# Kernel optimization log

Measured on AMD Instinct MI355X. Metric: run time of the kernel, lower is better.

## Reference

```python
import jax, jax.numpy as jnp
import numpy as np

B, L, D, H = 4, 2048, 2048, 16
HD = D // H
ROPE_BASE = 10000.0


def _rope_cos_sin(seq_len, dim):
    # torchtune-style: theta_i = base^{-2i/dim}, angles[t, i] = t * theta_i
    inv_freq = 1.0 / (ROPE_BASE ** (jnp.arange(0, dim, 2, dtype=jnp.float32) / dim))  # [dim/2]
    angles = jnp.arange(seq_len, dtype=jnp.float32)[:, None] * inv_freq[None, :]  # [L, dim/2]
    return jnp.cos(angles), jnp.sin(angles)


def _apply_rope(x, cos, sin):
    # x: [B, L, H, hd]; rotate interleaved pairs (x0, x1)
    x1 = x[..., 0::2]  # [B, L, H, hd/2]
    x2 = x[..., 1::2]
    c = cos[None, :, None, :]
    s = sin[None, :, None, :]
    o1 = x1 * c - x2 * s
    o2 = x2 * c + x1 * s
    return jnp.stack([o1, o2], axis=-1).reshape(x.shape)


def setup_inputs() -> dict:
    key = jax.random.key(0)
    k1, k2, k3 = jax.random.split(key, 3)
    x = jax.random.normal(k1, (B, L, D), dtype=jnp.float32)
    w_qkv = jax.random.normal(k2, (3 * D, D), dtype=jnp.float32) * (D ** -0.5)
    w_o = jax.random.normal(k3, (D, D), dtype=jnp.float32) * (D ** -0.5)
    return {"x": x, "w_qkv": w_qkv, "w_o": w_o}


def reference(x, w_qkv, w_o):
    qkv = jnp.einsum("bld,ed->ble", x, w_qkv)  # [B, L, 3D]
    q, k, v = jnp.split(qkv, 3, axis=-1)
    q = q.reshape(B, L, H, HD)
    k = k.reshape(B, L, H, HD)
    v = v.reshape(B, L, H, HD)
    cos, sin = _rope_cos_sin(L, HD)
    q = _apply_rope(q, cos, sin)
    k = _apply_rope(k, cos, sin)
    # [B, H, L, hd]
    q = q.transpose(0, 2, 1, 3)
    k = k.transpose(0, 2, 1, 3)
    v = v.transpose(0, 2, 1, 3)
    scores = jnp.einsum("bhqd,bhkd->bhqk", q, k) * (HD ** -0.5)
    causal = jnp.tril(jnp.ones((L, L), dtype=bool))
    scores = jnp.where(causal[None, None], scores, jnp.finfo(scores.dtype).min)
    attn = jax.nn.softmax(scores, axis=-1)
    y = jnp.einsum("bhqk,bhkd->bhqd", attn, v)
    y = y.transpose(0, 2, 1, 3).reshape(B, L, D)
    return jnp.einsum("bld,ed->ble", y, w_o)
```

## Files before the change

### kernel.cpp

```cpp
#include <hip/hip_runtime.h>

#define L_SEQ 2048
#define DMODEL 2048
#define NHEAD 16
#define HDIM 128
#define BATCH 4

typedef _Float16 f16x8 __attribute__((ext_vector_type(8)));
typedef _Float16 f16x4 __attribute__((ext_vector_type(4)));
typedef float f32x4 __attribute__((ext_vector_type(4)));

__device__ __forceinline__ void gload16(const void* g, void* l) {
  __builtin_amdgcn_global_load_lds((const __attribute__((address_space(1))) void*)g,
                                   (__attribute__((address_space(3))) void*)l, 16, 0, 0);
}

__global__ __launch_bounds__(256) void cvt_blocked(const float* __restrict__ in,
                                                   _Float16* __restrict__ out, int K) {
  const int kt = blockIdx.x, mb = blockIdx.y, KT = K >> 6;
  const int t = threadIdx.x, row = t >> 1, half = t & 1;
  const float* src = in + (size_t)(mb * 128 + row) * K + kt * 64 + half * 32;
  _Float16* tile = out + ((size_t)mb * KT + kt) * 8192;
  for (int j = 0; j < 4; ++j) {
    float4 a = *(const float4*)(src + j * 8);
    float4 b = *(const float4*)(src + j * 8 + 4);
    f16x8 o;
    o[0] = (_Float16)a.x; o[1] = (_Float16)a.y; o[2] = (_Float16)a.z; o[3] = (_Float16)a.w;
    o[4] = (_Float16)b.x; o[5] = (_Float16)b.y; o[6] = (_Float16)b.z; o[7] = (_Float16)b.w;
    int kb = half * 4 + j;
    *(f16x8*)(tile + (size_t)(kb * 128 + row) * 8) = o;
  }
}

template <typename OUT>
__global__ __launch_bounds__(256, 4) void gemm_bt(const _Float16* __restrict__ A,
                                                  const _Float16* __restrict__ Bt,
                                                  OUT* __restrict__ C,
                                                  int M, int N, int K) {
  __shared__ _Float16 As[2][128 * 64];
  __shared__ _Float16 Bs[2][128 * 64];
  const int KT = K >> 6;
  const int tid = threadIdx.x;
  const int wave = tid >> 6, lane = tid & 63, quad = lane >> 4, l15 = lane & 15;
  const int xcd = blockIdx.x & 7;
  const int lm = blockIdx.x >> 3;
  const int tm = xcd * 8 + (lm & 7);
  const int tn = lm >> 3;
  if (tm * 128 >= M || tn * 128 >= N) return;
  const int wm = (wave >> 1) * 64, wn = (wave & 1) * 64;
  const int id = wave * 4;
  const _Float16* tA0 = A + (size_t)tm * KT * 8192;
  const _Float16* tB0 = Bt + (size_t)tn * KT * 8192;

  auto stage = [&](int kt, int buf) {
    const _Float16* tA = tA0 + (size_t)kt * 8192;
    const _Float16* tB = tB0 + (size_t)kt * 8192;
    for (int j = 0; j < 4; ++j) {
      gload16(tA + (size_t)(id + j) * 512 + lane * 8, (char*)As[buf] + (id + j) * 1024);
      gload16(tB + (size_t)(id + j) * 512 + lane * 8, (char*)Bs[buf] + (id + j) * 1024);
    }
  };

  f32x4 acc[4][4] = {};
  stage(0, 0);
  int cur = 0;
  for (int kt = 0; kt < KT; ++kt) {
    const bool more = (kt + 1) < KT;
    if (more) {
      stage(kt + 1, cur ^ 1);
      asm volatile("s_waitcnt vmcnt(8)" ::: "memory");
    } else {
      asm volatile("s_waitcnt vmcnt(0)" ::: "memory");
    }
    __builtin_amdgcn_sched_barrier(0);
    __builtin_amdgcn_s_barrier();
    const f16x8* A8 = (const f16x8*)As[cur];
    const f16x8* B8 = (const f16x8*)Bs[cur];
    __builtin_amdgcn_s_setprio(1);
    for (int kk = 0; kk < 2; ++kk) {
      int kb = kk * 4 + quad;
      f16x8 af[4], bf[4];
      for (int mi = 0; mi < 4; ++mi) af[mi] = A8[kb * 128 + wm + mi * 16 + l15];
      for (int ni = 0; ni < 4; ++ni) bf[ni] = B8[kb * 128 + wn + ni * 16 + l15];
      for (int mi = 0; mi < 4; ++mi)
        for (int ni = 0; ni < 4; ++ni)
          acc[mi][ni] = __builtin_amdgcn_mfma_f32_16x16x32_f16(af[mi], bf[ni], acc[mi][ni], 0, 0, 0);
    }
    __builtin_amdgcn_s_setprio(0);
    asm volatile("s_waitcnt lgkmcnt(0)" ::: "memory");
    __builtin_amdgcn_sched_barrier(0);
    __builtin_amdgcn_s_barrier();
    cur ^= 1;
  }
  for (int mi = 0; mi < 4; ++mi)
    for (int ni = 0; ni < 4; ++ni) {
      int r = tm * 128 + wm + mi * 16 + quad * 4;
      int c = tn * 128 + wn + ni * 16 + l15;
      for (int reg = 0; reg < 4; ++reg)
        C[(size_t)(r + reg) * N + c] = (OUT)acc[mi][ni][reg];
    }
}

__global__ void rope_scatter(const _Float16* __restrict__ qkv,
                             _Float16* __restrict__ qt,
                             _Float16* __restrict__ kt) {
  int row = blockIdx.x;
  int pe = blockIdx.y * 256 + threadIdx.x;
  int e = pe * 2;
  float x1 = (float)qkv[(size_t)row * 6144 + e];
  float x2 = (float)qkv[(size_t)row * 6144 + e + 1];
  int which = e >> 11;
  int h = (e >> 7) & 15;
  int hd = e & 127;
  int b = row >> 11, l = row & 2047;
  int bh = b * 16 + h;
  int i = hd >> 1;
  float ang = (float)l * __expf((float)i * -0.14391156831212787f);
  float s, c;
  __sincosf(ang, &s, &c);
  float o1 = x1 * c - x2 * s;
  float o2 = x2 * c + x1 * s;
  _Float16* dst = (which == 0) ? qt : kt;
  size_t base = ((size_t)bh * 2048 + l) * 128 + hd;
  dst[base] = (_Float16)o1;
  dst[base + 1] = (_Float16)o2;
}

__global__ __launch_bounds__(256) void v_transpose(const _Float16* __restrict__ qkv,
                                                   _Float16* __restrict__ vt) {
  __shared__ _Float16 Ls[64 * 72];
  const int tid = threadIdx.x;
  const int l0 = blockIdx.x * 64;
  const int hd0 = blockIdx.y * 64;
  const int bh = blockIdx.z;
  const int b = bh >> 4, h = bh & 15;
  const size_t colbase = 4096 + h * 128 + hd0;
  for (int i = 0; i < 2; ++i) {
    int chunk = tid + i * 256;
    int r = chunk >> 3, c = chunk & 7;
    f16x8 v = *(const f16x8*)(qkv + (size_t)(b * 2048 + l0 + r) * 6144 + colbase + c * 8);
    *(f16x8*)(Ls + r * 72 + c * 8) = v;
  }
  __syncthreads();
  for (int i = 0; i < 2; ++i) {
    int chunk = tid + i * 256;
    int hr = chunk >> 3, c = chunk & 7;
    f16x8 o;
    for (int j = 0; j < 8; ++j) o[j] = Ls[(c * 8 + j) * 72 + hr];
    *(f16x8*)(vt + ((size_t)bh * 128 + hd0 + hr) * 2048 + l0 + c * 8) = o;
  }
}

__global__ __launch_bounds__(512, 4) void attn_fwd(const _Float16* __restrict__ qt,
                                                   const _Float16* __restrict__ kt,
                                                   const _Float16* __restrict__ vt,
                                                   _Float16* __restrict__ y) {
  __shared__ _Float16 Kl[64 * 128];
  __shared__ _Float16 Vl[64 * 128];
  __shared__ _Float16 Pl[8 * 16 * 64];
  const int a = blockIdx.y >> 2, bq = blockIdx.y & 3;
  const int qb = (a == 0) ? 15 - bq : (a == 1) ? 8 + bq : (a == 2) ? 4 + bq : 3 - bq;
  const int q0 = qb * 128;
  const int bh = blockIdx.x;
  const int tid = threadIdx.x;
  const int wave = tid >> 6, lane = tid & 63, quad = lane >> 4, l15 = lane & 15;
  const _Float16* Q = qt + (size_t)bh * L_SEQ * HDIM;
  const _Float16* Kg = kt + (size_t)bh * L_SEQ * HDIM;
  const _Float16* Vg = vt + (size_t)bh * HDIM * L_SEQ;

  const float scale = 0.08838834764831845f;
  f16x8 qf[4];
  {
    int qrow = q0 + wave * 16 + l15;
    const _Float16 hs = (_Float16)scale;
    for (int kk = 0; kk < 4; ++kk) {
      qf[kk] = *(const f16x8*)(Q + (size_t)qrow * 128 + kk * 32 + quad * 8);
      for (int j = 0; j < 8; ++j) qf[kk][j] *= hs;
    }
  }
  f32x4 o[8] = {};
  float mi[4] = {-1e30f, -1e30f, -1e30f, -1e30f};
  float li[4] = {0.f, 0.f, 0.f, 0.f};
  const int ntile = 2 * qb + 2;

  auto stageK = [&](int kv0) {
    for (int j = 0; j < 2; ++j) {
      int id = wave * 2 + j;
      gload16(Kg + (size_t)(kv0 + lane) * 128 + id * 8, (char*)Kl + id * 1024);
    }
  };
  auto stageV = [&](int kv0) {
    for (int j = 0; j < 2; ++j) {
      int id = wave * 2 + j;
      int kvb = id >> 1, h0 = (id & 1) * 64;
      gload16(Vg + (size_t)(h0 + lane) * L_SEQ + (kv0 + kvb * 8), (char*)Vl + (kvb * 128 + h0) * 16);
    }
  };

  stageK(0);
  stageV(0);

  for (int t = 0; t < ntile; ++t) {
    const int kv0 = t * 64;
    const bool more = (t + 1) < ntile;

    asm volatile("s_waitcnt vmcnt(2)" ::: "memory");
    __builtin_amdgcn_sched_barrier(0);
    __builtin_amdgcn_s_barrier();

    f32x4 s[4] = {};
    {
      const f16x8* K8 = (const f16x8*)Kl;
      __builtin_amdgcn_s_setprio(1);
      for (int kk = 0; kk < 4; ++kk) {
        int hb = kk * 4 + quad;
        for (int ni = 0; ni < 4; ++ni) {
          f16x8 bfr = K8[hb * 64 + ni * 16 + l15];
          s[ni] = __builtin_amdgcn_mfma_f32_16x16x32_f16(qf[kk], bfr, s[ni], 0, 0, 0);
        }
      }
      __builtin_amdgcn_s_setprio(0);
    }
    __builtin_amdgcn_sched_barrier(0);
    __builtin_amdgcn_s_barrier();
    __builtin_amdgcn_sched_barrier(0);
    if (more) stageK(kv0 + 64);

    float mx[4];
    if (t >= ntile - 2) {
      for (int reg = 0; reg < 4; ++reg) {
        int rowg = q0 + wave * 16 + quad * 4 + reg;
        float m = -1e30f;
        for (int ni = 0; ni < 4; ++ni) {
          float v = s[ni][reg];
          if ((kv0 + ni * 16 + l15) > rowg) v = -1e30f;
          s[ni][reg] = v;
          m = fmaxf(m, v);
        }
        mx[reg] = m;
      }
    } else {
      for (int reg = 0; reg < 4; ++reg)
        mx[reg] = fmaxf(fmaxf(s[0][reg], s[1][reg]), fmaxf(s[2][reg], s[3][reg]));
    }
    for (int off = 1; off < 16; off <<= 1)
      for (int reg = 0; reg < 4; ++reg)
        mx[reg] = fmaxf(mx[reg], __shfl_xor(mx[reg], off));
    float dm = fmaxf(fmaxf(mx[0] - mi[0], mx[1] - mi[1]),
                     fmaxf(mx[2] - mi[2], mx[3] - mi[3]));
    if (!__all(dm <= 8.0f)) {
      for (int reg = 0; reg < 4; ++reg) {
        float mn = fmaxf(mi[reg], mx[reg]);
        float al = __expf(mi[reg] - mn);
        mi[reg] = mn;
        li[reg] *= al;
        for (int ni = 0; ni < 8; ++ni) o[ni][reg] *= al;
      }
    }
    float rs[4] = {0.f, 0.f, 0.f, 0.f};
    _Float16* Pw = Pl + wave * (16 * 64);
    for (int ni = 0; ni < 4; ++ni) {
      int kv = ni * 16 + l15;
      int pbase = ((kv >> 3) * 16) * 8 + (kv & 7);
      for (int reg = 0; reg < 4; ++reg) {
        float p = __expf(s[ni][reg] - mi[reg]);
        rs[reg] += p;
        Pw[pbase + (quad * 4 + reg) * 8] = (_Float16)p;
      }
    }
    for (int off = 1; off < 16; off <<= 1)
      for (int reg = 0; reg < 4; ++reg)
        rs[reg] += __shfl_xor(rs[reg], off);
    for (int reg = 0; reg < 4; ++reg) li[reg] += rs[reg];

    if (more) {
      asm volatile("s_waitcnt vmcnt(2) lgkmcnt(0)" ::: "memory");
    } else {
      asm volatile("s_waitcnt vmcnt(0) lgkmcnt(0)" ::: "memory");
    }
    __builtin_amdgcn_sched_barrier(0);
    __builtin_amdgcn_s_barrier();

    {
      const f16x8* V8 = (const f16x8*)Vl;
      const f16x8* P8 = (const f16x8*)Pw;
      __builtin_amdgcn_s_setprio(1);
      for (int kk = 0; kk < 2; ++kk) {
        f16x8 pf = P8[(kk * 4 + quad) * 16 + l15];
        for (int ni = 0; ni < 8; ++ni) {
          f16x8 vf = V8[(kk * 4 + quad) * 128 + ni * 16 + l15];
          o[ni] = __builtin_amdgcn_mfma_f32_16x16x32_f16(pf, vf, o[ni], 0, 0, 0);
        }
      }
      __builtin_amdgcn_s_setprio(0);
    }
    __builtin_amdgcn_sched_barrier(0);
    __builtin_amdgcn_s_barrier();
    __builtin_amdgcn_sched_barrier(0);
    if (more) stageV(kv0 + 64);
  }
  int b = bh >> 4, h = bh & 15;
  for (int reg = 0; reg < 4; ++reg) {
    float inv = 1.f / li[reg];
    int gr = b * L_SEQ + q0 + wave * 16 + quad * 4 + reg;
    int mbt = gr >> 7, row = gr & 127;
    for (int ni = 0; ni < 8; ++ni) {
      int col = h * 128 + ni * 16 + l15;
      int cb = col >> 6, kb = (col >> 3) & 7, wi = col & 7;
      y[((size_t)mbt * 32 + cb) * 8192 + (size_t)(kb * 128 + row) * 8 + wi] =
          (_Float16)(o[ni][reg] * inv);
    }
  }
}

extern "C" void kernel_launch(void* const* d_in, const int* in_sizes, int n_in,
                              void* d_out, int out_size, void* d_ws, size_t ws_size,
                              hipStream_t stream) {
  const float* x = (const float*)d_in[0];
  const float* w_qkv = (const float*)d_in[1];
  const float* w_o = (const float*)d_in[2];
  float* out = (float*)d_out;

  char* ws = (char*)d_ws;
  _Float16* xb = (_Float16*)ws;    ws += (size_t)8192 * 2048 * 2;
  _Float16* wqkvb = (_Float16*)ws; ws += (size_t)6144 * 2048 * 2;
  _Float16* wob = (_Float16*)ws;   ws += (size_t)2048 * 2048 * 2;
  _Float16* qkv = (_Float16*)ws;   ws += (size_t)8192 * 6144 * 2;
  _Float16* qt = (_Float16*)ws;    ws += (size_t)64 * 2048 * 128 * 2;
  _Float16* kt = (_Float16*)ws;    ws += (size_t)64 * 2048 * 128 * 2;
  _Float16* vt = (_Float16*)ws;    ws += (size_t)64 * 2048 * 128 * 2;
  _Float16* y = qkv;

  cvt_blocked<<<dim3(32, 64), 256, 0, stream>>>(x, xb, 2048);
  cvt_blocked<<<dim3(32, 48), 256, 0, stream>>>(w_qkv, wqkvb, 2048);
  cvt_blocked<<<dim3(32, 16), 256, 0, stream>>>(w_o, wob, 2048);

  gemm_bt<_Float16><<<dim3(48 * 64), 256, 0, stream>>>(xb, wqkvb, qkv, 8192, 6144, 2048);
  rope_scatter<<<dim3(8192, 8), 256, 0, stream>>>(qkv, qt, kt);
  v_transpose<<<dim3(32, 2, 64), 256, 0, stream>>>(qkv, vt);
  attn_fwd<<<dim3(64, 16), 512, 0, stream>>>(qt, kt, vt, y);
  gemm_bt<float><<<dim3(16 * 64), 256, 0, stream>>>(y, wob, out, 8192, 2048, 2048);
}
```

Before: 649.0 us.

## Replace GEMM double buffer with single buffer refilled in halves

The GEMM's two full shared-memory stages for A and B become one 128x64 tile per operand, split into two k-halves. After a half is consumed, the next k-tile's copy of that half is issued while the other half is computed. This halves LDS use, from 64KB to 32KB per block, which may allow more resident blocks per CU. In exchange it adds an extra barrier per k-tile and leaves less prefetch distance to hide global-load latency.

After: 646.5 us. No clear change (-0.4%).

```diff
diff --git a/kernel.cpp b/kernel.cpp
--- a/kernel.cpp
+++ b/kernel.cpp
@@ -37,8 +37,8 @@
                                                   const _Float16* __restrict__ Bt,
                                                   OUT* __restrict__ C,
                                                   int M, int N, int K) {
-  __shared__ _Float16 As[2][128 * 64];
-  __shared__ _Float16 Bs[2][128 * 64];
+  __shared__ _Float16 As[128 * 64];
+  __shared__ _Float16 Bs[128 * 64];
   const int KT = K >> 6;
   const int tid = threadIdx.x;
   const int wave = tid >> 6, lane = tid & 63, quad = lane >> 4, l15 = lane & 15;
@@ -48,49 +48,52 @@
   const int tn = lm >> 3;
   if (tm * 128 >= M || tn * 128 >= N) return;
   const int wm = (wave >> 1) * 64, wn = (wave & 1) * 64;
-  const int id = wave * 4;
   const _Float16* tA0 = A + (size_t)tm * KT * 8192;
   const _Float16* tB0 = Bt + (size_t)tn * KT * 8192;
 
-  auto stage = [&](int kt, int buf) {
-    const _Float16* tA = tA0 + (size_t)kt * 8192;
-    const _Float16* tB = tB0 + (size_t)kt * 8192;
-    for (int j = 0; j < 4; ++j) {
-      gload16(tA + (size_t)(id + j) * 512 + lane * 8, (char*)As[buf] + (id + j) * 1024);
-      gload16(tB + (size_t)(id + j) * 512 + lane * 8, (char*)Bs[buf] + (id + j) * 1024);
+  auto stageH = [&](int kt, int h) {
+    const char* tA = (const char*)(tA0 + (size_t)kt * 8192);
+    const char* tB = (const char*)(tB0 + (size_t)kt * 8192);
+    for (int j = 0; j < 2; ++j) {
+      int off = h * 8192 + (wave * 2 + j) * 1024;
+      gload16(tA + off + lane * 16, (char*)As + off);
+      gload16(tB + off + lane * 16, (char*)Bs + off);
     }
   };
 
   f32x4 acc[4][4] = {};
-  stage(0, 0);
-  int cur = 0;
+  const f16x8* A8 = (const f16x8*)As;
+  const f16x8* B8 = (const f16x8*)Bs;
+
+  stageH(0, 0);
+  stageH(0, 1);
   for (int kt = 0; kt < KT; ++kt) {
     const bool more = (kt + 1) < KT;
-    if (more) {
-      stage(kt + 1, cur ^ 1);
-      asm volatile("s_waitcnt vmcnt(8)" ::: "memory");
-    } else {
-      asm volatile("s_waitcnt vmcnt(0)" ::: "memory");
-    }
-    __builtin_amdgcn_sched_barrier(0);
-    __builtin_amdgcn_s_barrier();
-    const f16x8* A8 = (const f16x8*)As[cur];
-    const f16x8* B8 = (const f16x8*)Bs[cur];
-    __builtin_amdgcn_s_setprio(1);
     for (int kk = 0; kk < 2; ++kk) {
-      int kb = kk * 4 + quad;
-      f16x8 af[4], bf[4];
-      for (int mi = 0; mi < 4; ++mi) af[mi] = A8[kb * 128 + wm + mi * 16 + l15];
-      for (int ni = 0; ni < 4; ++ni) bf[ni] = B8[kb * 128 + wn + ni * 16 + l15];
-      for (int mi = 0; mi < 4; ++mi)
-        for (int ni = 0; ni < 4; ++ni)
-          acc[mi][ni] = __builtin_amdgcn_mfma_f32_16x16x32_f16(af[mi], bf[ni], acc[mi][ni], 0, 0, 0);
-    }
-    __builtin_amdgcn_s_setprio(0);
-    asm volatile("s_waitcnt lgkmcnt(0)" ::: "memory");
-    __builtin_amdgcn_sched_barrier(0);
-    __builtin_amdgcn_s_barrier();
-    cur ^= 1;
+      if (kk == 0 || more) {
+        asm volatile("s_waitcnt vmcnt(4)" ::: "memory");
+      } else {
+        asm volatile("s_waitcnt vmcnt(0)" ::: "memory");
+      }
+      __builtin_amdgcn_sched_barrier(0);
+      __builtin_amdgcn_s_barrier();
+      {
+        int kb = kk * 4 + quad;
+        f16x8 af[4], bf[4];
+        for (int mi = 0; mi < 4; ++mi) af[mi] = A8[kb * 128 + wm + mi * 16 + l15];
+        for (int ni = 0; ni < 4; ++ni) bf[ni] = B8[kb * 128 + wn + ni * 16 + l15];
+        __builtin_amdgcn_s_setprio(1);
+        for (int mi = 0; mi < 4; ++mi)
+          for (int ni = 0; ni < 4; ++ni)
+            acc[mi][ni] = __builtin_amdgcn_mfma_f32_16x16x32_f16(af[mi], bf[ni], acc[mi][ni], 0, 0, 0);
+        __builtin_amdgcn_s_setprio(0);
+      }
+      asm volatile("s_waitcnt lgkmcnt(0)" ::: "memory");
+      __builtin_amdgcn_sched_barrier(0);
+      __builtin_amdgcn_s_barrier();
+      __builtin_amdgcn_sched_barrier(0);
+      if (more) stageH(kt + 1, kk);
+    }
   }
   for (int mi = 0; mi < 4; ++mi)
     for (int ni = 0; ni < 4; ++ni) {
```

## Enlarge GEMM tiles to 256x256 with 8-wave workgroups and remapped grid

Applied to the files above, without the earlier changes.

The shared GEMM kernel moves from 128x128 tiles with 4 waves to 256x256 tiles with 8 waves, each wave computing a 128x64 sub-tile. Each wave's accumulators double and every wave reuses its loaded B fragments across two A halves. The block-to-tile mapping changes to a per-XCD contiguous assignment, and the prefetch wait moves to the end of the iteration. This raises arithmetic intensity per LDS and global load, at the cost of higher register pressure, 128KB of LDS per workgroup, and far fewer workgroups (256 for the output projection), which risks underfilling the CUs.

New measurement: 647.3 us. About the same (-0.3%).

```diff
diff --git a/kernel.cpp b/kernel.cpp
--- a/kernel.cpp
+++ b/kernel.cpp
@@ -33,71 +33,73 @@
 }
 
 template <typename OUT>
-__global__ __launch_bounds__(256, 4) void gemm_bt(const _Float16* __restrict__ A,
+__global__ __launch_bounds__(512, 2) void gemm_bt(const _Float16* __restrict__ A,
                                                   const _Float16* __restrict__ Bt,
                                                   OUT* __restrict__ C,
                                                   int M, int N, int K) {
-  __shared__ _Float16 As[2][128 * 64];
-  __shared__ _Float16 Bs[2][128 * 64];
+  __shared__ _Float16 As[2][2][8192];
+  __shared__ _Float16 Bs[2][2][8192];
   const int KT = K >> 6;
   const int tid = threadIdx.x;
   const int wave = tid >> 6, lane = tid & 63, quad = lane >> 4, l15 = lane & 15;
-  const int xcd = blockIdx.x & 7;
-  const int lm = blockIdx.x >> 3;
-  const int tm = xcd * 8 + (lm & 7);
-  const int tn = lm >> 3;
-  if (tm * 128 >= M || tn * 128 >= N) return;
-  const int wm = (wave >> 1) * 64, wn = (wave & 1) * 64;
-  const int id = wave * 4;
-  const _Float16* tA0 = A + (size_t)tm * KT * 8192;
-  const _Float16* tB0 = Bt + (size_t)tn * KT * 8192;
-
-  auto stage = [&](int kt, int buf) {
-    const _Float16* tA = tA0 + (size_t)kt * 8192;
-    const _Float16* tB = tB0 + (size_t)kt * 8192;
-    for (int j = 0; j < 4; ++j) {
-      gload16(tA + (size_t)(id + j) * 512 + lane * 8, (char*)As[buf] + (id + j) * 1024);
-      gload16(tB + (size_t)(id + j) * 512 + lane * 8, (char*)Bs[buf] + (id + j) * 1024);
+  const int wr = wave >> 2, wc = wave & 3;
+  const int cpx = gridDim.x >> 3;
+  const int wgid = ((int)blockIdx.x & 7) * cpx + ((int)blockIdx.x >> 3);
+  const int MT = M >> 8;
+  const int tm = wgid % MT, tn = wgid / MT;
+
+  auto stage = [&](int t, int buf) {
+    for (int i = 0; i < 2; ++i) {
+      const char* srcA = (const char*)(A + ((size_t)(2 * tm + i) * KT + t) * 8192);
+      const char* srcB = (const char*)(Bt + ((size_t)(2 * tn + i) * KT + t) * 8192);
+      char* dstA = (char*)&As[buf][i][0];
+      char* dstB = (char*)&Bs[buf][i][0];
+      for (int j = 0; j < 2; ++j) {
+        int off = (wave * 2 + j) * 1024;
+        gload16(srcA + off + lane * 16, dstA + off);
+        gload16(srcB + off + lane * 16, dstB + off);
+      }
     }
   };
 
-  f32x4 acc[4][4] = {};
+  f32x4 acc[8][4] = {};
   stage(0, 0);
+  asm volatile("s_waitcnt vmcnt(0)" ::: "memory");
+  __builtin_amdgcn_sched_barrier(0);
+  __builtin_amdgcn_s_barrier();
   int cur = 0;
-  for (int kt = 0; kt < KT; ++kt) {
-    const bool more = (kt + 1) < KT;
-    if (more) {
-      stage(kt + 1, cur ^ 1);
-      asm volatile("s_waitcnt vmcnt(8)" ::: "memory");
-    } else {
-      asm volatile("s_waitcnt vmcnt(0)" ::: "memory");
-    }
-    __builtin_amdgcn_sched_barrier(0);
-    __builtin_amdgcn_s_barrier();
-    const f16x8* A8 = (const f16x8*)As[cur];
-    const f16x8* B8 = (const f16x8*)Bs[cur];
-    __builtin_amdgcn_s_setprio(1);
+  const int brow = (wc & 1) * 64;
+  for (int t = 0; t < KT; ++t) {
+    if (t + 1 < KT) stage(t + 1, cur ^ 1);
+    __builtin_amdgcn_sched_barrier(0);
+    const f16x8* A8 = (const f16x8*)&As[cur][wr][0];
+    const f16x8* B8 = (const f16x8*)&Bs[cur][wc >> 1][0];
     for (int kk = 0; kk < 2; ++kk) {
       int kb = kk * 4 + quad;
-      f16x8 af[4], bf[4];
-      for (int mi = 0; mi < 4; ++mi) af[mi] = A8[kb * 128 + wm + mi * 16 + l15];
-      for (int ni = 0; ni < 4; ++ni) bf[ni] = B8[kb * 128 + wn + ni * 16 + l15];
-      for (int mi = 0; mi < 4; ++mi)
-        for (int ni = 0; ni < 4; ++ni)
-          acc[mi][ni] = __builtin_amdgcn_mfma_f32_16x16x32_f16(af[mi], bf[ni], acc[mi][ni], 0, 0, 0);
-    }
-    __builtin_amdgcn_s_setprio(0);
-    asm volatile("s_waitcnt lgkmcnt(0)" ::: "memory");
+      f16x8 bf[4];
+      for (int ni = 0; ni < 4; ++ni) bf[ni] = B8[kb * 128 + brow + ni * 16 + l15];
+      for (int mh = 0; mh < 2; ++mh) {
+        f16x8 af[4];
+        for (int mi = 0; mi < 4; ++mi) af[mi] = A8[kb * 128 + mh * 64 + mi * 16 + l15];
+        __builtin_amdgcn_s_setprio(1);
+        for (int mi = 0; mi < 4; ++mi)
+          for (int ni = 0; ni < 4; ++ni)
+            acc[mh * 4 + mi][ni] =
+                __builtin_amdgcn_mfma_f32_16x16x32_f16(af[mi], bf[ni], acc[mh * 4 + mi][ni], 0, 0, 0);
+        __builtin_amdgcn_s_setprio(0);
+      }
+    }
+    asm volatile("s_waitcnt vmcnt(0)" ::: "memory");
     __builtin_amdgcn_sched_barrier(0);
     __builtin_amdgcn_s_barrier();
     cur ^= 1;
   }
-  for (int mi = 0; mi < 4; ++mi)
+  for (int a = 0; a < 8; ++a)
     for (int ni = 0; ni < 4; ++ni) {
-      int r = tm * 128 + wm + mi * 16 + quad * 4;
-      int c = tn * 128 + wn + ni * 16 + l15;
+      int r = tm * 256 + wr * 128 + (a >> 2) * 64 + (a & 3) * 16 + quad * 4;
+      int c = tn * 256 + wc * 64 + ni * 16 + l15;
       for (int reg = 0; reg < 4; ++reg)
-        C[(size_t)(r + reg) * N + c] = (OUT)acc[mi][ni][reg];
+        C[(size_t)(r + reg) * N + c] = (OUT)acc[a][ni][reg];
     }
 }
 
@@ -335,9 +337,9 @@
   cvt_blocked<<<dim3(32, 48), 256, 0, stream>>>(w_qkv, wqkvb, 2048);
   cvt_blocked<<<dim3(32, 16), 256, 0, stream>>>(w_o, wob, 2048);
 
-  gemm_bt<_Float16><<<dim3(48 * 64), 256, 0, stream>>>(xb, wqkvb, qkv, 8192, 6144, 2048);
+  gemm_bt<_Float16><<<dim3(768), 512, 0, stream>>>(xb, wqkvb, qkv, 8192, 6144, 2048);
   rope_scatter<<<dim3(8192, 8), 256, 0, stream>>>(qkv, qt, kt);
   v_transpose<<<dim3(32, 2, 64), 256, 0, stream>>>(qkv, vt);
   attn_fwd<<<dim3(64, 16), 512, 0, stream>>>(qt, kt, vt, y);
-  gemm_bt<float><<<dim3(16 * 64), 256, 0, stream>>>(y, wob, out, 8192, 2048, 2048);
-}
+  gemm_bt<float><<<dim3(256), 512, 0, stream>>>(y, wob, out, 8192, 2048, 2048);
+}
```
